# Kernel optimization log

Hardware: AMD Instinct MI355X
Metric: run time of the kernel (lower is better)

Reference implementation:

```python
import jax, jax.numpy as jnp
import numpy as np

N = 20000      # nodes
E = 320000     # edges (avg degree 16)
F_IN = 768
DIMS = [(768, 1536), (1536, 768), (768, 384), (384, 256), (256, 5)]


def setup_inputs() -> dict:
    key = jax.random.key(0)
    ks = jax.random.split(key, 2 + 3 * len(DIMS))
    inp = {
        'x': jax.random.normal(ks[0], (N, F_IN), dtype=jnp.float32),
        'edge_index': jax.random.randint(ks[1], (2, E), 0, N, dtype=jnp.int64),
    }
    for li, (fi, fo) in enumerate(DIMS):
        s = 1.0 / np.sqrt(fi)
        inp[f'Wl{li+1}'] = jax.random.uniform(ks[2 + 3 * li], (fi, fo), jnp.float32, -s, s)
        inp[f'Wr{li+1}'] = jax.random.uniform(ks[3 + 3 * li], (fi, fo), jnp.float32, -s, s)
        inp[f'b{li+1}'] = jax.random.uniform(ks[4 + 3 * li], (fo,), jnp.float32, -s, s)
    return inp


def _sage_conv(x, src, dst, deg_inv, Wl, Wr, b):
    # mean aggregate neighbor features, then linear (mean commutes with linear,
    # matching PyG SAGEConv which aggregates x_j then applies lin_l)
    agg = jax.ops.segment_sum(x[src], dst, num_segments=N) * deg_inv  # [N, F_in]
    return agg @ Wl + x @ Wr + b


def reference(x, edge_index,
              Wl1, Wr1, b1, Wl2, Wr2, b2, Wl3, Wr3, b3,
              Wl4, Wr4, b4, Wl5, Wr5, b5):
    src, dst = edge_index[0], edge_index[1]
    deg = jax.ops.segment_sum(jnp.ones((E,), jnp.float32), dst, num_segments=N)
    deg_inv = (1.0 / jnp.maximum(deg, 1.0))[:, None]  # clamp like PyG mean aggr

    h = jax.nn.relu(_sage_conv(x, src, dst, deg_inv, Wl1, Wr1, b1))
    h = jax.nn.relu(_sage_conv(h, src, dst, deg_inv, Wl2, Wr2, b2))
    h = jax.nn.relu(_sage_conv(h, src, dst, deg_inv, Wl3, Wr3, b3))
    h = jax.nn.relu(_sage_conv(h, src, dst, deg_inv, Wl4, Wr4, b4))  # [N, 256]
    out = _sage_conv(h, src, dst, deg_inv, Wl5, Wr5, b5)             # [N, 5]
    return (h, out)
```

## Files before the change

### kernel.cpp

```cpp
#include <hip/hip_runtime.h>
#include <stdint.h>

typedef __attribute__((ext_vector_type(8))) short short8;
typedef __attribute__((ext_vector_type(4))) float f32x4;

__device__ __forceinline__ float bf2f(unsigned short s) {
  return __uint_as_float(((unsigned)s) << 16);
}
__device__ __forceinline__ unsigned short f2bf(float f) {
  unsigned u = __float_as_uint(f);
  u += 0x7fffu + ((u >> 16) & 1u);
  return (unsigned short)(u >> 16);
}

__global__ void gs_count_deg(const int* __restrict__ dst, int* __restrict__ cnt, int E) {
  int e = blockIdx.x * 256 + threadIdx.x;
  if (e < E) atomicAdd(&cnt[dst[e]], 1);
}

__global__ void gs_scanA(const int* __restrict__ cnt, int* __restrict__ rp,
                         int* __restrict__ bsum, int n) {
  __shared__ int sm[256];
  const int b = blockIdx.x, t = threadIdx.x;
  const int base = b * 1024 + t * 4;
  int v[4]; int s = 0;
#pragma unroll
  for (int i = 0; i < 4; ++i) { v[i] = (base + i < n) ? cnt[base + i] : 0; s += v[i]; }
  sm[t] = s;
  __syncthreads();
  for (int off = 1; off < 256; off <<= 1) {
    int x = (t >= off) ? sm[t - off] : 0;
    __syncthreads();
    sm[t] += x;
    __syncthreads();
  }
  int run = sm[t] - s;
#pragma unroll
  for (int i = 0; i < 4; ++i) { if (base + i < n) rp[base + i] = run; run += v[i]; }
  if (t == 255) bsum[b] = sm[255];
}

__global__ void gs_scanC(int* __restrict__ rp, int* __restrict__ cur,
                         const int* __restrict__ bsum, int n, int nb) {
  __shared__ int sOff[65];
  const int t = threadIdx.x;
  if (t < 64) {
    int bv = (t < nb) ? bsum[t] : 0;
    int run = bv;
#pragma unroll
    for (int off = 1; off < 64; off <<= 1) {
      int x = __shfl_up(run, off, 64);
      if (t >= off) run += x;
    }
    sOff[t] = run - bv;
    if (t == 63) sOff[64] = run;
  }
  __syncthreads();
  int i = blockIdx.x * 256 + threadIdx.x;
  if (i < n) {
    int v = rp[i] + sOff[i >> 10];
    rp[i] = v;
    cur[i] = v;
  }
  if (i == n) rp[n] = sOff[64];
}

__global__ void gs_fill_csr(const int* __restrict__ src, const int* __restrict__ dst,
                            int* __restrict__ cur, int* __restrict__ col, int E) {
  int e = blockIdx.x * 256 + threadIdx.x;
  if (e < E) {
    int pos = atomicAdd(&cur[dst[e]], 1);
    col[pos] = src[e];
  }
}

__global__ void gs_f32_to_bf16(const float* __restrict__ in, unsigned short* __restrict__ out, int n4) {
  int i = blockIdx.x * 256 + threadIdx.x;
  if (i < n4) {
    float4 f = ((const float4*)in)[i];
    ushort4 o;
    o.x = f2bf(f.x); o.y = f2bf(f.y); o.z = f2bf(f.z); o.w = f2bf(f.w);
    ((ushort4*)out)[i] = o;
  }
}

struct TP { const float* W; unsigned short* WT; int K, F; };
struct TP8 { TP t[8]; };

__global__ void gs_tpack8(TP8 args) {
  const TP a = args.t[blockIdx.z];
  const int k0 = blockIdx.x * 32, f0 = blockIdx.y * 32;
  if (k0 >= a.K || f0 >= a.F) return;
  __shared__ float t[32][33];
  const int tx = threadIdx.x, ty = threadIdx.y;
#pragma unroll
  for (int r = ty; r < 32; r += 8) {
    int k = k0 + r, f = f0 + tx;
    t[r][tx] = (k < a.K && f < a.F) ? a.W[(size_t)k * a.F + f] : 0.f;
  }
  __syncthreads();
#pragma unroll
  for (int r = ty; r < 32; r += 8) {
    int f = f0 + r, k = k0 + tx;
    if (f < a.F && k < a.K) a.WT[(size_t)f * a.K + k] = f2bf(t[tx][r]);
  }
}

template<int VW>
__global__ __launch_bounds__(64)
void gs_agg_sliceT(const unsigned short* __restrict__ C, int ldc, int zoff,
                   const int* __restrict__ rp, const int* __restrict__ col,
                   const float* __restrict__ bias,
                   unsigned short* __restrict__ hout, float* __restrict__ fout,
                   int F, int relu) {
  const int v = blockIdx.x;
  const int l = threadIdx.x;
  const int cc = blockIdx.y * (64 * VW) + VW * l;
  const int s0 = rp[v], s1 = rp[v + 1];
  const float inv = 1.0f / (float)max(s1 - s0, 1);
  float a[VW];
#pragma unroll
  for (int q = 0; q < VW; ++q) a[q] = 0.f;

  auto accum = [&](int nrow) {
    const unsigned short* p = C + (size_t)nrow * ldc + cc;
    if constexpr (VW == 4) {
      ushort4 u = *(const ushort4*)p;
      a[0] += bf2f(u.x); a[1] += bf2f(u.y); a[2] += bf2f(u.z); a[3] += bf2f(u.w);
    } else {
      ushort2 u = *(const ushort2*)p;
      a[0] += bf2f(u.x); a[1] += bf2f(u.y);
    }
  };

  for (int base = s0; base < s1; base += 64) {
    int m = min(s1 - base, 64);
    int myNb = (l < m) ? col[base + l] : 0;
    int j = 0;
    for (; j + 4 <= m; j += 4) {
      int n0 = __shfl(myNb, j, 64);
      int n1 = __shfl(myNb, j + 1, 64);
      int n2 = __shfl(myNb, j + 2, 64);
      int n3 = __shfl(myNb, j + 3, 64);
      accum(n0); accum(n1); accum(n2); accum(n3);
    }
    for (; j < m; ++j) accum(__shfl(myNb, j, 64));
  }

  float o[VW];
#pragma unroll
  for (int q = 0; q < VW; ++q) o[q] = a[q] * inv;
  if (zoff >= 0) {
    const unsigned short* p = C + (size_t)v * ldc + zoff + cc;
    if constexpr (VW == 4) {
      ushort4 u = *(const ushort4*)p;
      o[0] += bf2f(u.x); o[1] += bf2f(u.y); o[2] += bf2f(u.z); o[3] += bf2f(u.w);
    } else {
      ushort2 u = *(const ushort2*)p;
      o[0] += bf2f(u.x); o[1] += bf2f(u.y);
    }
  }
  if (bias) {
#pragma unroll
    for (int q = 0; q < VW; ++q) o[q] += bias[cc + q];
  }
  if (relu) {
#pragma unroll
    for (int q = 0; q < VW; ++q) o[q] = fmaxf(o[q], 0.f);
  }
  if (hout) {
    if constexpr (VW == 4) {
      ushort4 u; u.x = f2bf(o[0]); u.y = f2bf(o[1]); u.z = f2bf(o[2]); u.w = f2bf(o[3]);
      *(ushort4*)(hout + (size_t)v * F + cc) = u;
    } else {
      ushort2 u; u.x = f2bf(o[0]); u.y = f2bf(o[1]);
      *(ushort2*)(hout + (size_t)v * F + cc) = u;
    }
  }
  if (fout) {
    if constexpr (VW == 4)
      *(float4*)(fout + (size_t)v * F + cc) = make_float4(o[0], o[1], o[2], o[3]);
    else
      *(float2*)(fout + (size_t)v * F + cc) = make_float2(o[0], o[1]);
  }
}

#define GLL(SRC, DST) __builtin_amdgcn_global_load_lds(                        \
    (const __attribute__((address_space(1))) unsigned int*)(SRC),              \
    (__attribute__((address_space(3))) unsigned int*)(DST), 16, 0, 0)

#define PHASE(T, MH, NH, RD_A, RD_B, ST_T, ST_B, ST_H, DO_VM)                  \
  {                                                                            \
    const int buf_ = (T) & 1;                                                  \
    if (RD_A) {                                                                \
      const unsigned short* Ab_ = &lA[buf_][MH][0];                            \
      _Pragma("unroll")                                                        \
      for (int fi = 0; fi < 4; ++fi) {                                         \
        int lra = wMl + fi * 16;                                               \
        _Pragma("unroll")                                                      \
        for (int ks = 0; ks < 2; ++ks) {                                       \
          int ch = (ks * 4 + qk) ^ (lra & 7);                                  \
          rA[fi][ks] = *(const short8*)&Ab_[lra * 64 + ch * 8];                \
        }                                                                      \
      }                                                                        \
    }                                                                          \
    if (RD_B) {                                                                \
      const unsigned short* Bb_ = &lB[buf_][NH][0];                            \
      _Pragma("unroll")                                                        \
      for (int fj = 0; fj < 2; ++fj) {                                         \
        int lrb = wNl + fj * 16;                                               \
        _Pragma("unroll")                                                      \
        for (int ks = 0; ks < 2; ++ks) {                                       \
          int ch = (ks * 4 + qk) ^ (lrb & 7);                                  \
          rB[NH][fj][ks] = *(const short8*)&Bb_[lrb * 64 + ch * 8];            \
        }                                                                      \
      }                                                                        \
    }                                                                          \
    STAGE(ST_T, ST_B, ST_H);                                                   \
    __builtin_amdgcn_s_setprio(1);                                             \
    _Pragma("unroll")                                                          \
    for (int fi = 0; fi < 4; ++fi)                                             \
      _Pragma("unroll")                                                        \
      for (int fj = 0; fj < 2; ++fj)                                           \
        _Pragma("unroll")                                                      \
        for (int ks = 0; ks < 2; ++ks)                                         \
          acc[MH][fi][NH][fj] = __builtin_amdgcn_mfma_f32_16x16x32_bf16(       \
              rA[fi][ks], rB[NH][fj][ks], acc[MH][fi][NH][fj], 0, 0, 0);       \
    __builtin_amdgcn_s_setprio(0);                                             \
    if (DO_VM) asm volatile("s_waitcnt vmcnt(4)" ::: "memory");                \
    asm volatile("s_barrier" ::: "memory");                                    \
  }

__global__ __launch_bounds__(512, 2)
void gs_gemm(const unsigned short* __restrict__ A1, const unsigned short* __restrict__ A2,
             const unsigned short* __restrict__ B1, const unsigned short* __restrict__ B2,
             const float* __restrict__ bias, unsigned short* __restrict__ Hout,
             int M, int Nn, int K, int doRelu, int Mt, int Nt) {
  __shared__ unsigned short lA[2][2][8192];
  __shared__ unsigned short lB[2][2][8192];
  const int tid = threadIdx.x;
  const int wid = tid >> 6;
  const int lane = tid & 63;

  const int MG = 8;
  const int per = MG * Nt;
  const int g = blockIdx.x / per;
  const int rem = blockIdx.x - g * per;
  const int gsz = min(MG, Mt - g * MG);
  const int nIdx = rem / gsz;
  const int mIdx = g * MG + (rem - nIdx * gsz);
  const int bM = mIdx * 256;
  const int bN = nIdx * 256;

  const int wM_ = wid >> 2;
  const int wN_ = wid & 3;
  const int qk  = lane >> 4;
  const int wMl = wM_ * 64 + (lane & 15);
  const int wNl = wN_ * 32 + (lane & 15);

  const int lr  = tid >> 3;
  const int swk = ((tid & 7) ^ (lr & 7)) * 8;
  const int rB0 = (lr >> 5) * 64 + (lr & 31);

  const int kt = K / 64;
  const int nt = A2 ? 2 * kt : kt;
  const int NI = nt / 2;

  f32x4 acc[2][4][2][2];
#pragma unroll
  for (int a = 0; a < 2; ++a)
#pragma unroll
    for (int b = 0; b < 4; ++b)
#pragma unroll
      for (int c = 0; c < 2; ++c)
#pragma unroll
        for (int d = 0; d < 2; ++d) acc[a][b][c][d] = (f32x4){0.f, 0.f, 0.f, 0.f};

  short8 rA[4][2];
  short8 rB[2][2][2];

  size_t offA[2][2], offB[2][2];
#pragma unroll
  for (int h = 0; h < 2; ++h) {
    int r1u = bM + h * 64 + lr;
    int r1 = (r1u < M) ? r1u : (M - 1);
    int r2u = r1u + 128;
    int r2 = (r2u < M) ? r2u : (M - 1);
    offA[h][0] = (size_t)r1 * K + swk;
    offA[h][1] = (size_t)r2 * K + swk;
    int rb = bN + h * 32 + rB0;
    offB[h][0] = (size_t)rb * K + swk;
    offB[h][1] = (size_t)(rb + 128) * K + swk;
  }

  auto STAGE = [&](int t, int isB, int h) {
    const int tc = (t < nt) ? t : (nt - 1);
    const int pass = (tc >= kt) ? 1 : 0;
    const int k0 = (tc - pass * kt) * 64;
    const int buf = t & 1;
    if (!isB) {
      const unsigned short* Ap = (pass ? A2 : A1) + k0;
      char* d = (char*)&lA[buf][h][0] + wid * 1024;
      GLL(Ap + offA[h][0], d);
      GLL(Ap + offA[h][1], d + 8192);
    } else {
      const unsigned short* Bp = (pass ? B2 : B1) + k0;
      char* d = (char*)&lB[buf][h][0] + wid * 1024;
      GLL(Bp + offB[h][0], d);
      GLL(Bp + offB[h][1], d + 8192);
    }
  };

  STAGE(0, 0, 0); STAGE(0, 1, 0); STAGE(0, 0, 1); STAGE(0, 1, 1);
  STAGE(1, 0, 0); STAGE(1, 1, 0);
  asm volatile("s_waitcnt vmcnt(4)" ::: "memory");
  asm volatile("s_barrier" ::: "memory");

  for (int i = 0; i < NI; ++i) {
    const int t0 = 2 * i, t1 = t0 + 1, t2 = t0 + 2, t3 = t0 + 3;
    PHASE(t0, 0, 0, 1, 1, t1, 0, 1, 0)
    PHASE(t0, 0, 1, 0, 1, t1, 1, 1, 0)
    PHASE(t0, 1, 0, 1, 0, t2, 0, 0, 0)
    PHASE(t0, 1, 1, 0, 0, t2, 1, 0, 1)
    PHASE(t1, 0, 0, 1, 1, t2, 0, 1, 0)
    PHASE(t1, 0, 1, 0, 1, t2, 1, 1, 0)
    PHASE(t1, 1, 0, 1, 0, t3, 0, 0, 0)
    PHASE(t1, 1, 1, 0, 0, t3, 1, 0, 1)
  }

#pragma unroll
  for (int mh = 0; mh < 2; ++mh)
#pragma unroll
    for (int fi = 0; fi < 4; ++fi) {
      const int row0 = bM + wM_ * 128 + mh * 64 + fi * 16 + (lane >> 4) * 4;
#pragma unroll
      for (int r = 0; r < 4; ++r) {
        const int row = row0 + r;
        if (row >= M) continue;
#pragma unroll
        for (int nh = 0; nh < 2; ++nh)
#pragma unroll
          for (int fj = 0; fj < 2; ++fj) {
            const int colN = bN + wN_ * 64 + nh * 32 + fj * 16 + (lane & 15);
            float v = acc[mh][fi][nh][fj][r];
            if (bias) v += bias[colN];
            if (doRelu) v = fmaxf(v, 0.f);
            Hout[(size_t)row * Nn + colN] = f2bf(v);
          }
      }
    }
}

__global__ __launch_bounds__(256)
void gs_l5dot(const unsigned short* __restrict__ h4, const float* __restrict__ Wl,
              const float* __restrict__ Wr, float* __restrict__ yz, int N) {
  __shared__ float sW[2560];
  const int t = threadIdx.x;
  for (int i = t; i < 2560; i += 256) sW[i] = (i < 1280) ? Wl[i] : Wr[i - 1280];
  __syncthreads();
  const int v = blockIdx.x * 4 + (t >> 6);
  if (v >= N) return;
  const int l = t & 63;
  ushort4 u = ((const ushort4*)(h4 + (size_t)v * 256))[l];
  float hv[4] = {bf2f(u.x), bf2f(u.y), bf2f(u.z), bf2f(u.w)};
  float acc[10];
#pragma unroll
  for (int n = 0; n < 10; ++n) acc[n] = 0.f;
#pragma unroll
  for (int tt = 0; tt < 4; ++tt) {
    int k = 4 * l + tt;
#pragma unroll
    for (int n = 0; n < 5; ++n) {
      acc[n] += hv[tt] * sW[k * 5 + n];
      acc[5 + n] += hv[tt] * sW[1280 + k * 5 + n];
    }
  }
#pragma unroll
  for (int n = 0; n < 10; ++n)
    for (int off = 32; off > 0; off >>= 1) acc[n] += __shfl_down(acc[n], off, 64);
  if (l == 0) {
#pragma unroll
    for (int n = 0; n < 10; ++n) yz[(size_t)v * 10 + n] = acc[n];
  }
}

__global__ __launch_bounds__(256)
void gs_l5agg(const float* __restrict__ yz, const int* __restrict__ rp,
              const int* __restrict__ col, const float* __restrict__ b,
              float* __restrict__ out, int N) {
  const int t = threadIdx.x;
  const int v = blockIdx.x * 16 + (t >> 4);
  if (v >= N) return;
  const int l = t & 15;
  const int s0 = rp[v], s1 = rp[v + 1];
  const float inv = 1.0f / (float)max(s1 - s0, 1);
  float acc[5] = {0.f, 0.f, 0.f, 0.f, 0.f};
  for (int e = s0 + l; e < s1; e += 16) {
    const float* yr = yz + (size_t)col[e] * 10;
#pragma unroll
    for (int n = 0; n < 5; ++n) acc[n] += yr[n];
  }
#pragma unroll
  for (int n = 0; n < 5; ++n) {
    acc[n] += __shfl_down(acc[n], 8, 16);
    acc[n] += __shfl_down(acc[n], 4, 16);
    acc[n] += __shfl_down(acc[n], 2, 16);
    acc[n] += __shfl_down(acc[n], 1, 16);
  }
  if (l == 0) {
#pragma unroll
    for (int n = 0; n < 5; ++n)
      out[(size_t)v * 5 + n] = acc[n] * inv + yz[(size_t)v * 10 + 5 + n] + b[n];
  }
}

extern "C" void kernel_launch(void* const* d_in, const int* in_sizes, int n_in,
                              void* d_out, int out_size, void* d_ws, size_t ws_size,
                              hipStream_t stream) {
  const float* x = (const float*)d_in[0];
  const int* ei = (const int*)d_in[1];
  const int N = in_sizes[0] / 768;
  const int E = in_sizes[1] / 2;
  const int* src = ei;
  const int* dst = ei + E;

  const float* Wl[5];
  const float* Wr[5];
  const float* bb[5];
  for (int l = 0; l < 5; ++l) {
    Wl[l] = (const float*)d_in[2 + 3 * l];
    Wr[l] = (const float*)d_in[3 + 3 * l];
    bb[l] = (const float*)d_in[4 + 3 * l];
  }

  char* w = (char*)d_ws;
  size_t off = 0;
  auto take = [&](size_t bytes) -> char* {
    char* p = w + off;
    off = (off + bytes + 255) & ~(size_t)255;
    return p;
  };
  unsigned short* ar1 = (unsigned short*)take((size_t)N * 768 * 2);
  unsigned short* ar2 = (unsigned short*)take((size_t)N * 768 * 2);
  unsigned short* ar3 = (unsigned short*)take((size_t)N * 1536 * 2);
  unsigned short* C2  = (unsigned short*)take((size_t)N * 1536 * 2);
  int* cnt  = (int*)take((size_t)N * 4);
  int* rp   = (int*)take((size_t)(N + 1) * 4);
  int* cur  = (int*)take((size_t)N * 4);
  int* col  = (int*)take((size_t)E * 4);
  const int nbChunks = (N + 1023) / 1024;
  int* bsum = (int*)take((size_t)(nbChunks + 1) * 4);
  unsigned short* WT1l = (unsigned short*)take((size_t)1536 * 768 * 2);
  unsigned short* WT1r = (unsigned short*)take((size_t)1536 * 768 * 2);
  unsigned short* WT2  = (unsigned short*)take((size_t)1536 * 1536 * 2);
  unsigned short* WT3  = (unsigned short*)take((size_t)768 * 768 * 2);
  unsigned short* WT4  = (unsigned short*)take((size_t)512 * 384 * 2);

  unsigned short* xb   = ar1;
  unsigned short* C3   = ar1;
  unsigned short* aggb = ar2;
  unsigned short* h2   = ar2;
  unsigned short* h1   = ar3;
  unsigned short* C4   = ar3;
  unsigned short* h3   = ar3 + (size_t)N * 512;
  unsigned short* h4   = ar3 + (size_t)N * (512 + 384);
  float*          yz5  = (float*)(ar3 + (size_t)N * (512 + 384 + 256));

  const int M = N;
  const int Mt = (M + 255) / 256;

  hipMemsetAsync(cnt, 0, (size_t)N * 4, stream);
  gs_count_deg<<<(E + 255) / 256, 256, 0, stream>>>(dst, cnt, E);
  gs_scanA<<<nbChunks, 256, 0, stream>>>(cnt, rp, bsum, N);
  gs_scanC<<<(N + 256) / 256, 256, 0, stream>>>(rp, cur, bsum, N, nbChunks);
  gs_fill_csr<<<(E + 255) / 256, 256, 0, stream>>>(src, dst, cur, col, E);

  gs_f32_to_bf16<<<((N * 768 / 4) + 255) / 256, 256, 0, stream>>>(x, xb, N * 768 / 4);
  TP8 tp;
  tp.t[0] = {Wl[0], WT1l, 768, 1536};
  tp.t[1] = {Wr[0], WT1r, 768, 1536};
  tp.t[2] = {Wl[1], WT2, 1536, 768};
  tp.t[3] = {Wr[1], WT2 + (size_t)768 * 1536, 1536, 768};
  tp.t[4] = {Wl[2], WT3, 768, 384};
  tp.t[5] = {Wr[2], WT3 + (size_t)384 * 768, 768, 384};
  tp.t[6] = {Wl[3], WT4, 384, 256};
  tp.t[7] = {Wr[3], WT4 + (size_t)256 * 384, 384, 256};
  gs_tpack8<<<dim3(48, 48, 8), dim3(32, 8), 0, stream>>>(tp);

  float* houtF = (float*)d_out;
  float* out5  = (float*)d_out + (size_t)N * 256;

  gs_agg_sliceT<4><<<dim3(N, 3), 64, 0, stream>>>(xb, 768, -1, rp, col, nullptr, aggb, nullptr, 768, 0);
  gs_gemm<<<Mt * 6, 512, 0, stream>>>(aggb, xb, WT1l, WT1r, bb[0], h1, M, 1536, 768, 1, Mt, 6);

  gs_gemm<<<Mt * 6, 512, 0, stream>>>(h1, nullptr, WT2, nullptr, nullptr, C2, M, 1536, 1536, 0, Mt, 6);
  gs_agg_sliceT<4><<<dim3(N, 3), 64, 0, stream>>>(C2, 1536, 768, rp, col, bb[1], h2, nullptr, 768, 1);

  gs_gemm<<<Mt * 3, 512, 0, stream>>>(h2, nullptr, WT3, nullptr, nullptr, C3, M, 768, 768, 0, Mt, 3);
  gs_agg_sliceT<2><<<dim3(N, 3), 64, 0, stream>>>(C3, 768, 384, rp, col, bb[2], h3, nullptr, 384, 1);

  gs_gemm<<<Mt * 2, 512, 0, stream>>>(h3, nullptr, WT4, nullptr, nullptr, C4, M, 512, 384, 0, Mt, 2);
  gs_agg_sliceT<4><<<dim3(N, 1), 64, 0, stream>>>(C4, 512, 256, rp, col, bb[3], h4, houtF, 256, 1);

  gs_l5dot<<<(N + 3) / 4, 256, 0, stream>>>(h4, Wl[4], Wr[4], yz5, N);
  gs_l5agg<<<(N + 15) / 16, 256, 0, stream>>>(yz5, rp, col, bb[4], out5, N);
}
```

Baseline: 653.4 us.

## Shrink GEMM tiles to 128x128 with 256 threads and fuse prep kernels

The GEMM kernel moves from 256x256 tiles with 512 threads to 128x128 tiles with 256 threads. The LDS buffers, staging offsets, warp layout and phase schedule are reworked to match, and the grid is roughly quadrupled. The intent is better CU occupancy and load balance for M=20000, at the cost of less data reuse per tile. The bf16 conversion of x, the degree count and the weight transpose are also merged into one prep launch to cut kernel-launch overhead.

Measured after the change: 726.4 us. 1.11x slower.

```diff
diff --git a/kernel.cpp b/kernel.cpp
--- a/kernel.cpp
+++ b/kernel.cpp
@@ -11,11 +11,6 @@
   unsigned u = __float_as_uint(f);
   u += 0x7fffu + ((u >> 16) & 1u);
   return (unsigned short)(u >> 16);
-}
-
-__global__ void gs_count_deg(const int* __restrict__ dst, int* __restrict__ cnt, int E) {
-  int e = blockIdx.x * 256 + threadIdx.x;
-  if (e < E) atomicAdd(&cnt[dst[e]], 1);
 }
 
 __global__ void gs_scanA(const int* __restrict__ cnt, int* __restrict__ rp,
@@ -74,35 +69,49 @@
   }
 }
 
-__global__ void gs_f32_to_bf16(const float* __restrict__ in, unsigned short* __restrict__ out, int n4) {
-  int i = blockIdx.x * 256 + threadIdx.x;
-  if (i < n4) {
-    float4 f = ((const float4*)in)[i];
-    ushort4 o;
-    o.x = f2bf(f.x); o.y = f2bf(f.y); o.z = f2bf(f.z); o.w = f2bf(f.w);
-    ((ushort4*)out)[i] = o;
-  }
-}
-
 struct TP { const float* W; unsigned short* WT; int K, F; };
 struct TP8 { TP t[8]; };
 
-__global__ void gs_tpack8(TP8 args) {
-  const TP a = args.t[blockIdx.z];
-  const int k0 = blockIdx.x * 32, f0 = blockIdx.y * 32;
+__global__ __launch_bounds__(256)
+void gs_prep(const float* __restrict__ x, unsigned short* __restrict__ xb, int n4,
+             const int* __restrict__ dst, int* __restrict__ cnt, int E,
+             TP8 args) {
+  __shared__ float tb[32][33];
+  const int nConv = (n4 + 255) >> 8;
+  const int nDeg = (E + 255) >> 8;
+  int bid = blockIdx.x;
+  if (bid < nConv) {
+    int i = bid * 256 + threadIdx.x;
+    if (i < n4) {
+      float4 f = ((const float4*)x)[i];
+      ushort4 o;
+      o.x = f2bf(f.x); o.y = f2bf(f.y); o.z = f2bf(f.z); o.w = f2bf(f.w);
+      ((ushort4*)xb)[i] = o;
+    }
+    return;
+  }
+  bid -= nConv;
+  if (bid < nDeg) {
+    int e = bid * 256 + threadIdx.x;
+    if (e < E) atomicAdd(&cnt[dst[e]], 1);
+    return;
+  }
+  bid -= nDeg;
+  const TP a = args.t[bid / (48 * 48)];
+  const int rem = bid % (48 * 48);
+  const int k0 = (rem % 48) * 32, f0 = (rem / 48) * 32;
   if (k0 >= a.K || f0 >= a.F) return;
-  __shared__ float t[32][33];
-  const int tx = threadIdx.x, ty = threadIdx.y;
+  const int tx = threadIdx.x & 31, ty = threadIdx.x >> 5;
 #pragma unroll
   for (int r = ty; r < 32; r += 8) {
     int k = k0 + r, f = f0 + tx;
-    t[r][tx] = (k < a.K && f < a.F) ? a.W[(size_t)k * a.F + f] : 0.f;
+    tb[r][tx] = (k < a.K && f < a.F) ? a.W[(size_t)k * a.F + f] : 0.f;
   }
   __syncthreads();
 #pragma unroll
   for (int r = ty; r < 32; r += 8) {
     int f = f0 + r, k = k0 + tx;
-    if (f < a.F && k < a.K) a.WT[(size_t)f * a.K + k] = f2bf(t[tx][r]);
+    if (f < a.F && k < a.K) a.WT[(size_t)f * a.K + k] = f2bf(tb[tx][r]);
   }
 }
 
@@ -195,7 +204,7 @@
     if (RD_A) {                                                                \
       const unsigned short* Ab_ = &lA[buf_][MH][0];                            \
       _Pragma("unroll")                                                        \
-      for (int fi = 0; fi < 4; ++fi) {                                         \
+      for (int fi = 0; fi < 2; ++fi) {                                         \
         int lra = wMl + fi * 16;                                               \
         _Pragma("unroll")                                                      \
         for (int ks = 0; ks < 2; ++ks) {                                       \
@@ -219,7 +228,7 @@
     STAGE(ST_T, ST_B, ST_H);                                                   \
     __builtin_amdgcn_s_setprio(1);                                             \
     _Pragma("unroll")                                                          \
-    for (int fi = 0; fi < 4; ++fi)                                             \
+    for (int fi = 0; fi < 2; ++fi)                                             \
       _Pragma("unroll")                                                        \
       for (int fj = 0; fj < 2; ++fj)                                           \
         _Pragma("unroll")                                                      \
@@ -231,13 +240,13 @@
     asm volatile("s_barrier" ::: "memory");                                    \
   }
 
-__global__ __launch_bounds__(512, 2)
+__global__ __launch_bounds__(256, 2)
 void gs_gemm(const unsigned short* __restrict__ A1, const unsigned short* __restrict__ A2,
              const unsigned short* __restrict__ B1, const unsigned short* __restrict__ B2,
              const float* __restrict__ bias, unsigned short* __restrict__ Hout,
              int M, int Nn, int K, int doRelu, int Mt, int Nt) {
-  __shared__ unsigned short lA[2][2][8192];
-  __shared__ unsigned short lB[2][2][8192];
+  __shared__ unsigned short lA[2][2][4096];
+  __shared__ unsigned short lB[2][2][4096];
   const int tid = threadIdx.x;
   const int wid = tid >> 6;
   const int lane = tid & 63;
@@ -249,34 +258,32 @@
   const int gsz = min(MG, Mt - g * MG);
   const int nIdx = rem / gsz;
   const int mIdx = g * MG + (rem - nIdx * gsz);
-  const int bM = mIdx * 256;
-  const int bN = nIdx * 256;
-
-  const int wM_ = wid >> 2;
-  const int wN_ = wid & 3;
+  const int bM = mIdx * 128;
+  const int bN = nIdx * 128;
+
+  const int wM_ = wid >> 1;
+  const int wN_ = wid & 1;
   const int qk  = lane >> 4;
-  const int wMl = wM_ * 64 + (lane & 15);
+  const int wMl = wM_ * 32 + (lane & 15);
   const int wNl = wN_ * 32 + (lane & 15);
 
   const int lr  = tid >> 3;
   const int swk = ((tid & 7) ^ (lr & 7)) * 8;
-  const int rB0 = (lr >> 5) * 64 + (lr & 31);
 
   const int kt = K / 64;
   const int nt = A2 ? 2 * kt : kt;
-  const int NI = nt / 2;
-
-  f32x4 acc[2][4][2][2];
+
+  f32x4 acc[2][2][2][2];
 #pragma unroll
   for (int a = 0; a < 2; ++a)
 #pragma unroll
-    for (int b = 0; b < 4; ++b)
+    for (int b = 0; b < 2; ++b)
 #pragma unroll
       for (int c = 0; c < 2; ++c)
 #pragma unroll
         for (int d = 0; d < 2; ++d) acc[a][b][c][d] = (f32x4){0.f, 0.f, 0.f, 0.f};
 
-  short8 rA[4][2];
+  short8 rA[2][2];
   short8 rB[2][2][2];
 
   size_t offA[2][2], offB[2][2];
@@ -284,13 +291,13 @@
   for (int h = 0; h < 2; ++h) {
     int r1u = bM + h * 64 + lr;
     int r1 = (r1u < M) ? r1u : (M - 1);
-    int r2u = r1u + 128;
+    int r2u = r1u + 32;
     int r2 = (r2u < M) ? r2u : (M - 1);
     offA[h][0] = (size_t)r1 * K + swk;
     offA[h][1] = (size_t)r2 * K + swk;
-    int rb = bN + h * 32 + rB0;
+    int rb = bN + h * 64 + lr;
     offB[h][0] = (size_t)rb * K + swk;
-    offB[h][1] = (size_t)(rb + 128) * K + swk;
+    offB[h][1] = (size_t)(rb + 32) * K + swk;
   }
 
   auto STAGE = [&](int t, int isB, int h) {
@@ -302,37 +309,32 @@
       const unsigned short* Ap = (pass ? A2 : A1) + k0;
       char* d = (char*)&lA[buf][h][0] + wid * 1024;
       GLL(Ap + offA[h][0], d);
-      GLL(Ap + offA[h][1], d + 8192);
+      GLL(Ap + offA[h][1], d + 4096);
     } else {
       const unsigned short* Bp = (pass ? B2 : B1) + k0;
       char* d = (char*)&lB[buf][h][0] + wid * 1024;
       GLL(Bp + offB[h][0], d);
-      GLL(Bp + offB[h][1], d + 8192);
+      GLL(Bp + offB[h][1], d + 4096);
     }
   };
 
-  STAGE(0, 0, 0); STAGE(0, 1, 0); STAGE(0, 0, 1); STAGE(0, 1, 1);
+  STAGE(0, 0, 0); STAGE(0, 1, 0); STAGE(0, 1, 1); STAGE(0, 0, 1);
   STAGE(1, 0, 0); STAGE(1, 1, 0);
   asm volatile("s_waitcnt vmcnt(4)" ::: "memory");
   asm volatile("s_barrier" ::: "memory");
 
-  for (int i = 0; i < NI; ++i) {
-    const int t0 = 2 * i, t1 = t0 + 1, t2 = t0 + 2, t3 = t0 + 3;
-    PHASE(t0, 0, 0, 1, 1, t1, 0, 1, 0)
-    PHASE(t0, 0, 1, 0, 1, t1, 1, 1, 0)
-    PHASE(t0, 1, 0, 1, 0, t2, 0, 0, 0)
-    PHASE(t0, 1, 1, 0, 0, t2, 1, 0, 1)
-    PHASE(t1, 0, 0, 1, 1, t2, 0, 1, 0)
-    PHASE(t1, 0, 1, 0, 1, t2, 1, 1, 0)
-    PHASE(t1, 1, 0, 1, 0, t3, 0, 0, 0)
-    PHASE(t1, 1, 1, 0, 0, t3, 1, 0, 1)
+  for (int t = 0; t < nt; ++t) {
+    PHASE(t, 0, 0, 1, 1, t + 1, 1, 1, 0)
+    PHASE(t, 0, 1, 0, 1, t + 1, 0, 1, 0)
+    PHASE(t, 1, 0, 1, 0, t + 2, 0, 0, 0)
+    PHASE(t, 1, 1, 0, 0, t + 2, 1, 0, 1)
   }
 
 #pragma unroll
   for (int mh = 0; mh < 2; ++mh)
 #pragma unroll
-    for (int fi = 0; fi < 4; ++fi) {
-      const int row0 = bM + wM_ * 128 + mh * 64 + fi * 16 + (lane >> 4) * 4;
+    for (int fi = 0; fi < 2; ++fi) {
+      const int row0 = bM + mh * 64 + wM_ * 32 + fi * 16 + (lane >> 4) * 4;
 #pragma unroll
       for (int r = 0; r < 4; ++r) {
         const int row = row0 + r;
@@ -341,7 +343,7 @@
         for (int nh = 0; nh < 2; ++nh)
 #pragma unroll
           for (int fj = 0; fj < 2; ++fj) {
-            const int colN = bN + wN_ * 64 + nh * 32 + fj * 16 + (lane & 15);
+            const int colN = bN + nh * 64 + wN_ * 32 + fj * 16 + (lane & 15);
             float v = acc[mh][fi][nh][fj][r];
             if (bias) v += bias[colN];
             if (doRelu) v = fmaxf(v, 0.f);
@@ -467,15 +469,9 @@
   float*          yz5  = (float*)(ar3 + (size_t)N * (512 + 384 + 256));
 
   const int M = N;
-  const int Mt = (M + 255) / 256;
+  const int Mt = (M + 127) / 128;
 
   hipMemsetAsync(cnt, 0, (size_t)N * 4, stream);
-  gs_count_deg<<<(E + 255) / 256, 256, 0, stream>>>(dst, cnt, E);
-  gs_scanA<<<nbChunks, 256, 0, stream>>>(cnt, rp, bsum, N);
-  gs_scanC<<<(N + 256) / 256, 256, 0, stream>>>(rp, cur, bsum, N, nbChunks);
-  gs_fill_csr<<<(E + 255) / 256, 256, 0, stream>>>(src, dst, cur, col, E);
-
-  gs_f32_to_bf16<<<((N * 768 / 4) + 255) / 256, 256, 0, stream>>>(x, xb, N * 768 / 4);
   TP8 tp;
   tp.t[0] = {Wl[0], WT1l, 768, 1536};
   tp.t[1] = {Wr[0], WT1r, 768, 1536};
@@ -485,21 +481,27 @@
   tp.t[5] = {Wr[2], WT3 + (size_t)384 * 768, 768, 384};
   tp.t[6] = {Wl[3], WT4, 384, 256};
   tp.t[7] = {Wr[3], WT4 + (size_t)256 * 384, 384, 256};
-  gs_tpack8<<<dim3(48, 48, 8), dim3(32, 8), 0, stream>>>(tp);
+  const int n4 = N * 768 / 4;
+  const int prepBlocks = ((n4 + 255) >> 8) + ((E + 255) >> 8) + 48 * 48 * 8;
+  gs_prep<<<prepBlocks, 256, 0, stream>>>(x, xb, n4, dst, cnt, E, tp);
+
+  gs_scanA<<<nbChunks, 256, 0, stream>>>(cnt, rp, bsum, N);
+  gs_scanC<<<(N + 256) / 256, 256, 0, stream>>>(rp, cur, bsum, N, nbChunks);
+  gs_fill_csr<<<(E + 255) / 256, 256, 0, stream>>>(src, dst, cur, col, E);
 
   float* houtF = (float*)d_out;
   float* out5  = (float*)d_out + (size_t)N * 256;
 
   gs_agg_sliceT<4><<<dim3(N, 3), 64, 0, stream>>>(xb, 768, -1, rp, col, nullptr, aggb, nullptr, 768, 0);
-  gs_gemm<<<Mt * 6, 512, 0, stream>>>(aggb, xb, WT1l, WT1r, bb[0], h1, M, 1536, 768, 1, Mt, 6);
-
-  gs_gemm<<<Mt * 6, 512, 0, stream>>>(h1, nullptr, WT2, nullptr, nullptr, C2, M, 1536, 1536, 0, Mt, 6);
+  gs_gemm<<<Mt * 12, 256, 0, stream>>>(aggb, xb, WT1l, WT1r, bb[0], h1, M, 1536, 768, 1, Mt, 12);
+
+  gs_gemm<<<Mt * 12, 256, 0, stream>>>(h1, nullptr, WT2, nullptr, nullptr, C2, M, 1536, 1536, 0, Mt, 12);
   gs_agg_sliceT<4><<<dim3(N, 3), 64, 0, stream>>>(C2, 1536, 768, rp, col, bb[1], h2, nullptr, 768, 1);
 
-  gs_gemm<<<Mt * 3, 512, 0, stream>>>(h2, nullptr, WT3, nullptr, nullptr, C3, M, 768, 768, 0, Mt, 3);
+  gs_gemm<<<Mt * 6, 256, 0, stream>>>(h2, nullptr, WT3, nullptr, nullptr, C3, M, 768, 768, 0, Mt, 6);
   gs_agg_sliceT<2><<<dim3(N, 3), 64, 0, stream>>>(C3, 768, 384, rp, col, bb[2], h3, nullptr, 384, 1);
 
-  gs_gemm<<<Mt * 2, 512, 0, stream>>>(h3, nullptr, WT4, nullptr, nullptr, C4, M, 512, 384, 0, Mt, 2);
+  gs_gemm<<<Mt * 4, 256, 0, stream>>>(h3, nullptr, WT4, nullptr, nullptr, C4, M, 512, 384, 0, Mt, 4);
   gs_agg_sliceT<4><<<dim3(N, 1), 64, 0, stream>>>(C4, 512, 256, rp, col, bb[3], h4, houtF, 256, 1);
 
   gs_l5dot<<<(N + 3) / 4, 256, 0, stream>>>(h4, Wl[4], Wr[4], yz5, N);
```
